# Kernel optimization log

Hardware: AMD Instinct MI355X
Metric: run time of the kernel (lower is better)

The kernel has to match this reference:

```python
import jax, jax.numpy as jnp
import numpy as np

N_NODES = 50000
N_EDGES = 800000
N_ENT = 500000
N_REL = 500
L = 2          # num_layers
H = 8          # head_num
D = 16         # per-head dim (hidden_dim // head_num)
HID = H * D    # 128
IN = 128       # in_ent_dim == in_rel_dim == hidden_dim
B = 64         # number of graphs in the batch
SLOPE = 0.2    # leaky-relu negative slope


def setup_inputs() -> dict:
    key = jax.random.key(0)
    ks = jax.random.split(key, 11)
    return {
        "ent_table": jax.random.normal(ks[0], (N_ENT, IN), jnp.float32) * 0.05,
        "rel_table": jax.random.normal(ks[1], (N_REL, IN), jnp.float32) * 0.05,
        "W_ent": jax.random.normal(ks[2], (L, IN, HID), jnp.float32) * 0.05,
        "W_rel": jax.random.normal(ks[3], (L, IN, HID), jnp.float32) * 0.05,
        "attn_l": jax.random.normal(ks[4], (L, H, D), jnp.float32) * 0.05,
        "attn_r": jax.random.normal(ks[5], (L, H, D), jnp.float32) * 0.05,
        "attn_e": jax.random.normal(ks[6], (L, H, D), jnp.float32) * 0.05,
        "ent_ids": jax.random.randint(ks[7], (N_NODES,), 0, N_ENT, jnp.int32),
        "rel_ids": jax.random.randint(ks[8], (N_EDGES,), 0, N_REL, jnp.int32),
        "src": jax.random.randint(ks[9], (N_EDGES,), 0, N_NODES, jnp.int32),
        "dst": jax.random.randint(ks[10], (N_EDGES,), 0, N_NODES, jnp.int32),
        # node-0 offset of each subgraph in the batched graph
        "graph_offsets": jnp.arange(B, dtype=jnp.int32) * (N_NODES // B),
    }


def _kge_layer(h, rel_f, src, dst, W_e, W_r, a_l, a_r, a_e):
    # GAT-style relation-aware message passing (KGELayer)
    feat = (h @ W_e).reshape(-1, H, D)        # [N,H,D]
    rfeat = (rel_f @ W_r).reshape(-1, H, D)   # [E,H,D]
    el = jnp.einsum('nhd,hd->nh', feat, a_l)  # src score
    er = jnp.einsum('nhd,hd->nh', feat, a_r)  # dst score
    ee = jnp.einsum('ehd,hd->eh', rfeat, a_e) # relation score
    e = jax.nn.leaky_relu(el[src] + er[dst] + ee, SLOPE)  # [E,H]
    # segment softmax over incoming edges of each dst node
    emax = jax.ops.segment_max(e, dst, num_segments=N_NODES)
    ex = jnp.exp(e - emax[dst])
    denom = jax.ops.segment_sum(ex, dst, num_segments=N_NODES)
    alpha = ex / denom[dst]                   # [E,H]
    msg = (feat[src] + rfeat) * alpha[:, :, None]  # [E,H,D]
    out = jax.ops.segment_sum(msg, dst, num_segments=N_NODES)  # [N,H,D]
    return out.reshape(-1, HID)


def reference(ent_table, rel_table, W_ent, W_rel, attn_l, attn_r, attn_e,
              ent_ids, rel_ids, src, dst, graph_offsets):
    h = ent_table[ent_ids]       # [N,IN]
    rel_f = rel_table[rel_ids]   # [E,IN]
    for l in range(L):
        h = _kge_layer(h, rel_f, src, dst, W_ent[l], W_rel[l],
                       attn_l[l], attn_r[l], attn_e[l])
    # CLS embedding: node 0 of each unbatched subgraph
    return h[graph_offsets]      # [B,HID]
```

## Files before the change

kernel.cpp:

```cpp
#include <hip/hip_runtime.h>
#include <hip/hip_bf16.h>


#define NN   50000
#define NE   800000
#define NR   500
#define HH   8
#define DD   16
#define HIDD 128
#define BB   64

#define MAXE2 16384
#define MAXS1 16448
#define MAXE1 262144
#define MAXS0 50000


__global__ void k_init(int* slot2, int* slot1, int* slot0, int* counters) {
    int i = blockIdx.x * blockDim.x + threadIdx.x;
    int stride = gridDim.x * blockDim.x;
    for (int n = i; n < NN; n += stride) { slot2[n] = -1; slot1[n] = -1; slot0[n] = -1; }
    if (i < 8) counters[i] = 0;
}

__global__ void k_seed(const int* goffs, int* slot2, int* slot1, int* nodesS1,
                       int* counters) {
    int i = threadIdx.x;
    if (i < BB) {
        int n = goffs[i];
        slot2[n] = i;
        slot1[n] = -2;
        nodesS1[i] = n;
    }
    if (i == 0) counters[0] = BB;
}

#define EBUF 1024
#define NBUF 512
__global__ void k_scan(const int* __restrict__ src, const int* __restrict__ dst,
                       const int* __restrict__ slotHit, int* __restrict__ slotNew,
                       int* elist, int elistCap, int* nodes, int nodesCap,
                       int* counters, int cntE, int cntN) {
    __shared__ int lE[EBUF];
    __shared__ int lN[NBUF];
    __shared__ int cEsh, cNsh, baseE, baseN;
    if (threadIdx.x == 0) { cEsh = 0; cNsh = 0; }
    __syncthreads();
    int per = (NE + gridDim.x - 1) / gridDim.x;
    int lo = blockIdx.x * per;
    int hi = lo + per; if (hi > NE) hi = NE;
    for (int base = lo; base < hi; base += blockDim.x) {
        int e = base + threadIdx.x;
        if (e < hi) {
            int d = dst[e];
            if (slotHit[d] >= 0) {
                int pos = atomicAdd(&cEsh, 1);
                lE[pos] = e;
                int s = src[e];
                int old = atomicCAS(&slotNew[s], -1, -2);
                if (old == -1) {
                    int p2 = atomicAdd(&cNsh, 1);
                    lN[p2] = s;
                }
            }
        }
        __syncthreads();
        if (cEsh >= EBUF - 256 || cNsh >= NBUF - 256) {
            int nE = cEsh, nN = cNsh;
            if (threadIdx.x == 0) {
                baseE = atomicAdd(&counters[cntE], nE);
                baseN = atomicAdd(&counters[cntN], nN);
            }
            __syncthreads();
            for (int i = threadIdx.x; i < nE; i += blockDim.x) {
                int g = baseE + i; if (g < elistCap) elist[g] = lE[i];
            }
            for (int i = threadIdx.x; i < nN; i += blockDim.x) {
                int g = baseN + i; if (g < nodesCap) nodes[g] = lN[i];
            }
            __syncthreads();
            if (threadIdx.x == 0) { cEsh = 0; cNsh = 0; }
        }
        __syncthreads();
    }
    int nE = cEsh, nN = cNsh;
    if (threadIdx.x == 0) {
        baseE = atomicAdd(&counters[cntE], nE);
        baseN = atomicAdd(&counters[cntN], nN);
    }
    __syncthreads();
    for (int i = threadIdx.x; i < nE; i += blockDim.x) {
        int g = baseE + i; if (g < elistCap) elist[g] = lE[i];
    }
    for (int i = threadIdx.x; i < nN; i += blockDim.x) {
        int g = baseN + i; if (g < nodesCap) nodes[g] = lN[i];
    }
}

__global__ void k_finS1(int* slot1, const int* nodesS1, int* slot0, int* nodesS0,
                        int* counters, int* deg) {
    int k = blockIdx.x * blockDim.x + threadIdx.x;
    int cnt = counters[0]; if (cnt > MAXS1) cnt = MAXS1;
    if (k < cnt) {
        int n = nodesS1[k];
        slot1[n] = k;
        slot0[n] = -2;
        nodesS0[k] = n;
    }
    if (k < MAXS1) deg[k] = 0;
    if (k == 0) counters[1] = cnt;
}

__global__ void k_finS0(int* slot0, const int* nodesS0, const int* counters) {
    int k = blockIdx.x * blockDim.x + threadIdx.x;
    int cnt = counters[1]; if (cnt > MAXS0) cnt = MAXS0;
    if (k < cnt) slot0[nodesS0[k]] = k;
}


__global__ void k_deg(const int* e1list, const int* counters, const int* dst,
                      const int* slot1, int* deg) {
    int i = blockIdx.x * blockDim.x + threadIdx.x;
    int stride = gridDim.x * blockDim.x;
    int cnt = counters[3]; if (cnt > MAXE1) cnt = MAXE1;
    for (; i < cnt; i += stride) {
        int e = e1list[i];
        atomicAdd(&deg[slot1[dst[e]]], 1);
    }
}

#define PFXT 1024
__global__ void k_pfx(const int* counters, const int* __restrict__ deg,
                      int* rowstart, int* cursor) {
    __shared__ int buf[PFXT];
    __shared__ int carrySh;
    int t = threadIdx.x;
    int cnt = counters[0]; if (cnt > MAXS1) cnt = MAXS1;
    if (t == 0) carrySh = 0;
    __syncthreads();
    for (int base = 0; base < cnt; base += PFXT) {
        int i = base + t;
        int v = (i < cnt) ? deg[i] : 0;
        buf[t] = v;
        __syncthreads();
        for (int off = 1; off < PFXT; off <<= 1) {
            int x = (t >= off) ? buf[t - off] : 0;
            __syncthreads();
            buf[t] += x;
            __syncthreads();
        }
        int carry = carrySh;
        int excl = carry + buf[t] - v;
        if (i < cnt) { rowstart[i] = excl; cursor[i] = excl; }
        __syncthreads();
        if (t == PFXT - 1) carrySh = carry + buf[PFXT - 1];
        __syncthreads();
    }
    if (t == 0) rowstart[cnt] = carrySh;
}

__global__ void k_bucket(const int* e1list, const int* counters, const int* dst,
                         const int* slot1, int* cursor, int* ebuck) {
    int i = blockIdx.x * blockDim.x + threadIdx.x;
    int stride = gridDim.x * blockDim.x;
    int cnt = counters[3]; if (cnt > MAXE1) cnt = MAXE1;
    for (; i < cnt; i += stride) {
        int e = e1list[i];
        int kd = slot1[dst[e]];
        int pos = atomicAdd(&cursor[kd], 1);
        ebuck[pos] = e;
    }
}

__global__ void k_rel(const float* rel_table, const float* __restrict__ W_rel,
                      const float* attn_e, float* rproj, float* ee) {
    int b = blockIdx.x;
    int l = b / NR, r = b % NR;
    int t = threadIdx.x;
    __shared__ float row[HIDD];
    __shared__ float rp[HIDD];
    row[t] = rel_table[r * HIDD + t];
    __syncthreads();
    const float* W = W_rel + l * HIDD * HIDD;
    float acc = 0.f;
    for (int j = 0; j < HIDD; j++) acc += row[j] * W[j * HIDD + t];
    rproj[(l * NR + r) * HIDD + t] = acc;
    rp[t] = acc;
    __syncthreads();
    if (t < HH) {
        float s = 0.f;
        for (int d = 0; d < DD; d++) s += rp[t * DD + d] * attn_e[(l * HH + t) * DD + d];
        ee[(l * NR + r) * HH + t] = s;
    }
}

#define FT 8
__global__ void k_feat0(const int* nodesS0, const int* counters, const int* ent_ids,
                        const float* __restrict__ ent_table, const float* __restrict__ W_ent,
                        const float* __restrict__ attn_l, const float* __restrict__ attn_r,
                        float* feat0, float* el0, float* er0) {
    int t = threadIdx.x;
    int cnt = counters[1]; if (cnt > MAXS0) cnt = MAXS0;
    __shared__ float rows[FT][HIDD];
    int nTiles = (cnt + FT - 1) / FT;
    for (int tile = blockIdx.x; tile < nTiles; tile += gridDim.x) {
        int k0 = tile * FT;
        #pragma unroll
        for (int m = 0; m < FT; m++) {
            int k = k0 + m;
            int n = nodesS0[k < cnt ? k : 0];
            rows[m][t] = ent_table[(long)ent_ids[n] * HIDD + t];
        }
        __syncthreads();
        float acc[FT];
        #pragma unroll
        for (int m = 0; m < FT; m++) acc[m] = 0.f;
        for (int j = 0; j < HIDD; j++) {
            float w = W_ent[j * HIDD + t];
            #pragma unroll
            for (int m = 0; m < FT; m++) acc[m] += rows[m][j] * w;
        }
        __syncthreads();
        #pragma unroll
        for (int m = 0; m < FT; m++) {
            int k = k0 + m;
            if (k < cnt) feat0[k * HIDD + t] = acc[m];
            rows[m][t] = acc[m];
        }
        __syncthreads();
        {
            int m = t >> 4, idx = t & 15, h = idx >> 1, isR = idx & 1;
            int k = k0 + m;
            if (k < cnt) {
                const float* av = (isR ? attn_r : attn_l) + h * DD;
                float s = 0.f;
                for (int d = 0; d < DD; d++) s += rows[m][h * DD + d] * av[d];
                if (isR) er0[k * HH + h] = s; else el0[k * HH + h] = s;
            }
        }
        __syncthreads();
    }
}

__global__ void k_layer1(const int* counters, const int* nodesS1,
                         const int* __restrict__ rowstart, const int* __restrict__ ebuck,
                         const int* __restrict__ src, const int* __restrict__ rel_ids,
                         const int* __restrict__ slot0,
                         const float* __restrict__ feat0, const float* __restrict__ rproj0,
                         const float* __restrict__ el0, const float* __restrict__ er0,
                         const float* __restrict__ ee0,
                         const float* __restrict__ W_ent1,
                         const float* attn_l1, const float* attn_r1,
                         float* feat1, float* el1, float* er1) {
    int t = threadIdx.x;
    int h = t >> 4;
    int cnt = counters[0]; if (cnt > MAXS1) cnt = MAXS1;
    __shared__ float row[HIDD];
    __shared__ float f[HIDD];
    for (int k = blockIdx.x; k < cnt; k += gridDim.x) {
        int n = nodesS1[k];
        int kd0 = slot0[n];
        float er_h = er0[kd0 * HH + h];
        int lo = rowstart[k], hi = rowstart[k + 1];
        float acc = 0.f, den = 0.f;
        for (int i = lo; i < hi; i++) {
            int e = ebuck[i];
            int s = src[e];
            int ks = slot0[s];
            int rid = rel_ids[e];
            float sc = el0[ks * HH + h] + er_h + ee0[rid * HH + h];
            sc = sc >= 0.f ? sc : 0.2f * sc;
            float ex = expf(sc);
            acc += (feat0[ks * HIDD + t] + rproj0[rid * HIDD + t]) * ex;
            den += ex;
        }
        row[t] = den > 0.f ? acc / den : 0.f;
        __syncthreads();
        float a2 = 0.f;
        for (int j = 0; j < HIDD; j++) a2 += row[j] * W_ent1[j * HIDD + t];
        feat1[k * HIDD + t] = a2;
        f[t] = a2;
        __syncthreads();
        if (t < HH) {
            float s = 0.f;
            for (int d = 0; d < DD; d++) s += f[t * DD + d] * attn_l1[t * DD + d];
            el1[k * HH + t] = s;
        } else if (t < 2 * HH) {
            int hh = t - HH;
            float s = 0.f;
            for (int d = 0; d < DD; d++) s += f[hh * DD + d] * attn_r1[hh * DD + d];
            er1[k * HH + hh] = s;
        }
        __syncthreads();
    }
}

__global__ void k_layer2(const int* counters, const int* goffs,
                         const int* __restrict__ e2list,
                         const int* __restrict__ src, const int* __restrict__ dst,
                         const int* __restrict__ rel_ids,
                         const int* __restrict__ slot1, const int* __restrict__ slot2,
                         const float* __restrict__ feat1, const float* __restrict__ rproj1,
                         const float* __restrict__ el1, const float* __restrict__ er1,
                         const float* __restrict__ ee1,
                         float* out) {
    int g = blockIdx.x;
    int t = threadIdx.x;
    int h = t >> 4;
    int cnt2 = counters[2]; if (cnt2 > MAXE2) cnt2 = MAXE2;
    int n = goffs[g];
    int kd1 = slot1[n];
    float er_h = er1[kd1 * HH + h];
    __shared__ int lE[128];
    __shared__ int lc;
    float acc = 0.f, den = 0.f;
    for (int base = 0; base < cnt2; base += blockDim.x) {
        if (t == 0) lc = 0;
        __syncthreads();
        int i = base + t;
        if (i < cnt2) {
            int e = e2list[i];
            if (slot2[dst[e]] == g) {
                int p = atomicAdd(&lc, 1);
                lE[p] = e;
            }
        }
        __syncthreads();
        int m = lc;
        for (int q = 0; q < m; q++) {
            int e = lE[q];
            int s = src[e];
            int ks = slot1[s];
            int rid = rel_ids[e];
            float sc = el1[ks * HH + h] + er_h + ee1[rid * HH + h];
            sc = sc >= 0.f ? sc : 0.2f * sc;
            float ex = expf(sc);
            acc += (feat1[ks * HIDD + t] + rproj1[rid * HIDD + t]) * ex;
            den += ex;
        }
        __syncthreads();
    }
    out[g * HIDD + t] = den > 0.f ? acc / den : 0.f;
}

extern "C" void kernel_launch(void* const* d_in, const int* in_sizes, int n_in,
                              void* d_out, int out_size, void* d_ws, size_t ws_size,
                              hipStream_t stream) {
    const float* ent_table = (const float*)d_in[0];
    const float* rel_table = (const float*)d_in[1];
    const float* W_ent     = (const float*)d_in[2];
    const float* W_rel     = (const float*)d_in[3];
    const float* attn_l    = (const float*)d_in[4];
    const float* attn_r    = (const float*)d_in[5];
    const float* attn_e    = (const float*)d_in[6];
    const int*   ent_ids   = (const int*)d_in[7];
    const int*   rel_ids   = (const int*)d_in[8];
    const int*   src       = (const int*)d_in[9];
    const int*   dst       = (const int*)d_in[10];
    const int*   goffs     = (const int*)d_in[11];
    float*       out       = (float*)d_out;

    char* p = (char*)d_ws;
    auto alloc = [&](size_t nbytes) {
        void* q = (void*)p;
        p += (nbytes + 255) & ~(size_t)255;
        return q;
    };
    float* rproj   = (float*)alloc((size_t)2 * NR * HIDD * 4);
    float* ee      = (float*)alloc((size_t)2 * NR * HH * 4);
    int*   slot2   = (int*)alloc((size_t)NN * 4);
    int*   slot1   = (int*)alloc((size_t)NN * 4);
    int*   slot0   = (int*)alloc((size_t)NN * 4);
    int*   nodesS1 = (int*)alloc((size_t)MAXS1 * 4);
    int*   nodesS0 = (int*)alloc((size_t)MAXS0 * 4);
    int*   e2list  = (int*)alloc((size_t)MAXE2 * 4);
    int*   e1list  = (int*)alloc((size_t)MAXE1 * 4);
    int*   counters= (int*)alloc(8 * 4);
    int*   deg     = (int*)alloc((size_t)MAXS1 * 4);
    int*   rowstart= (int*)alloc((size_t)(MAXS1 + 1) * 4);
    int*   cursor  = (int*)alloc((size_t)MAXS1 * 4);
    int*   ebuck   = (int*)alloc((size_t)MAXE1 * 4);
    float* feat0   = (float*)alloc((size_t)MAXS0 * HIDD * 4);
    float* el0     = (float*)alloc((size_t)MAXS0 * HH * 4);
    float* er0     = (float*)alloc((size_t)MAXS0 * HH * 4);
    float* feat1   = (float*)alloc((size_t)MAXS1 * HIDD * 4);
    float* el1     = (float*)alloc((size_t)MAXS1 * HH * 4);
    float* er1     = (float*)alloc((size_t)MAXS1 * HH * 4);

    const float* rproj0 = rproj;
    const float* rproj1 = rproj + (size_t)NR * HIDD;
    const float* ee0 = ee;
    const float* ee1 = ee + (size_t)NR * HH;
    const float* W_ent0 = W_ent;
    const float* W_ent1 = W_ent + HIDD * HIDD;
    const float* attn_l0 = attn_l, *attn_l1 = attn_l + HH * DD;
    const float* attn_r0 = attn_r, *attn_r1 = attn_r + HH * DD;

    hipLaunchKernelGGL(k_init, dim3(256), dim3(256), 0, stream,
                       slot2, slot1, slot0, counters);
    hipLaunchKernelGGL(k_seed, dim3(1), dim3(64), 0, stream,
                       goffs, slot2, slot1, nodesS1, counters);
    hipLaunchKernelGGL(k_scan, dim3(512), dim3(256), 0, stream,
                       src, dst, slot2, slot1, e2list, MAXE2, nodesS1, MAXS1,
                       counters, 2, 0);
    hipLaunchKernelGGL(k_finS1, dim3((MAXS1 + 255) / 256), dim3(256), 0, stream,
                       slot1, nodesS1, slot0, nodesS0, counters, deg);
    hipLaunchKernelGGL(k_scan, dim3(512), dim3(256), 0, stream,
                       src, dst, slot1, slot0, e1list, MAXE1, nodesS0, MAXS0,
                       counters, 3, 1);
    hipLaunchKernelGGL(k_finS0, dim3((MAXS0 + 255) / 256), dim3(256), 0, stream,
                       slot0, nodesS0, counters);
    hipLaunchKernelGGL(k_deg, dim3(256), dim3(256), 0, stream,
                       e1list, counters, dst, slot1, deg);
    hipLaunchKernelGGL(k_pfx, dim3(1), dim3(PFXT), 0, stream,
                       counters, deg, rowstart, cursor);
    hipLaunchKernelGGL(k_bucket, dim3(256), dim3(256), 0, stream,
                       e1list, counters, dst, slot1, cursor, ebuck);
    hipLaunchKernelGGL(k_rel, dim3(2 * NR), dim3(HIDD), 0, stream,
                       rel_table, W_rel, attn_e, rproj, ee);
    hipLaunchKernelGGL(k_feat0, dim3(1024), dim3(HIDD), 0, stream,
                       nodesS0, counters, ent_ids, ent_table, W_ent0,
                       attn_l0, attn_r0, feat0, el0, er0);
    hipLaunchKernelGGL(k_layer1, dim3(2048), dim3(HIDD), 0, stream,
                       counters, nodesS1, rowstart, ebuck, src, rel_ids, slot0,
                       feat0, rproj0, el0, er0, ee0, W_ent1, attn_l1, attn_r1,
                       feat1, el1, er1);
    hipLaunchKernelGGL(k_layer2, dim3(BB), dim3(HIDD), 0, stream,
                       counters, goffs, e2list, src, dst, rel_ids, slot1, slot2,
                       feat1, rproj1, el1, er1, ee1, out);
}
```

Baseline: 455.7 us.

## Bucket edges into fixed-capacity per-node slots during scan, fuse setup kernels

The frontier scan now writes each matching edge straight into a fixed-stride per-destination bucket using an atomic cursor. This removes the edge list, degree count, prefix sum and bucketing kernels. The relation projection, layer-0 feature projection and slot0 finalisation are fused into one launch. Both layer kernels precompute source slots, relation ids and exp scores per edge in shared memory before the aggregation loop. The fixed capacity of 256 edges per node silently drops edges beyond that, and contention on the global per-slot atomics may rise.

```diff
diff --git a/kernel.cpp b/kernel.cpp
--- a/kernel.cpp
+++ b/kernel.cpp
@@ -10,16 +10,19 @@
 #define HIDD 128
 #define BB   64
 
-#define MAXE2 16384
 #define MAXS1 16448
-#define MAXE1 262144
 #define MAXS0 50000
-
-
-__global__ void k_init(int* slot2, int* slot1, int* slot0, int* counters) {
+#define MAXD1 256
+#define MAXD2 256
+
+
+__global__ void k_init(int* slot2, int* slot1, int* slot0, int* c1, int* c2,
+                       int* counters) {
     int i = blockIdx.x * blockDim.x + threadIdx.x;
     int stride = gridDim.x * blockDim.x;
     for (int n = i; n < NN; n += stride) { slot2[n] = -1; slot1[n] = -1; slot0[n] = -1; }
+    for (int n = i; n < MAXS1; n += stride) c1[n] = 0;
+    if (i < BB) c2[i] = 0;
     if (i < 8) counters[i] = 0;
 }
 
@@ -35,16 +38,14 @@
     if (i == 0) counters[0] = BB;
 }
 
-#define EBUF 1024
 #define NBUF 512
 __global__ void k_scan(const int* __restrict__ src, const int* __restrict__ dst,
                        const int* __restrict__ slotHit, int* __restrict__ slotNew,
-                       int* elist, int elistCap, int* nodes, int nodesCap,
-                       int* counters, int cntE, int cntN) {
-    __shared__ int lE[EBUF];
+                       int* __restrict__ ebuck, int maxd, int* __restrict__ cursor,
+                       int* nodes, int nodesCap, int* counters, int cntN) {
     __shared__ int lN[NBUF];
-    __shared__ int cEsh, cNsh, baseE, baseN;
-    if (threadIdx.x == 0) { cEsh = 0; cNsh = 0; }
+    __shared__ int cNsh, baseN;
+    if (threadIdx.x == 0) cNsh = 0;
     __syncthreads();
     int per = (NE + gridDim.x - 1) / gridDim.x;
     int lo = blockIdx.x * per;
@@ -53,9 +54,10 @@
         int e = base + threadIdx.x;
         if (e < hi) {
             int d = dst[e];
-            if (slotHit[d] >= 0) {
-                int pos = atomicAdd(&cEsh, 1);
-                lE[pos] = e;
+            int slot = slotHit[d];
+            if (slot >= 0) {
+                int pos = atomicAdd(&cursor[slot], 1);
+                if (pos < maxd) ebuck[slot * maxd + pos] = e;
                 int s = src[e];
                 int old = atomicCAS(&slotNew[s], -1, -2);
                 if (old == -1) {
@@ -65,40 +67,28 @@
             }
         }
         __syncthreads();
-        if (cEsh >= EBUF - 256 || cNsh >= NBUF - 256) {
-            int nE = cEsh, nN = cNsh;
-            if (threadIdx.x == 0) {
-                baseE = atomicAdd(&counters[cntE], nE);
-                baseN = atomicAdd(&counters[cntN], nN);
-            }
+        if (cNsh >= NBUF - 256) {
+            int nN = cNsh;
+            if (threadIdx.x == 0) baseN = atomicAdd(&counters[cntN], nN);
             __syncthreads();
-            for (int i = threadIdx.x; i < nE; i += blockDim.x) {
-                int g = baseE + i; if (g < elistCap) elist[g] = lE[i];
-            }
             for (int i = threadIdx.x; i < nN; i += blockDim.x) {
                 int g = baseN + i; if (g < nodesCap) nodes[g] = lN[i];
             }
             __syncthreads();
-            if (threadIdx.x == 0) { cEsh = 0; cNsh = 0; }
-        }
-        __syncthreads();
-    }
-    int nE = cEsh, nN = cNsh;
-    if (threadIdx.x == 0) {
-        baseE = atomicAdd(&counters[cntE], nE);
-        baseN = atomicAdd(&counters[cntN], nN);
-    }
+            if (threadIdx.x == 0) cNsh = 0;
+        }
+        __syncthreads();
+    }
+    int nN = cNsh;
+    if (threadIdx.x == 0) baseN = atomicAdd(&counters[cntN], nN);
     __syncthreads();
-    for (int i = threadIdx.x; i < nE; i += blockDim.x) {
-        int g = baseE + i; if (g < elistCap) elist[g] = lE[i];
-    }
     for (int i = threadIdx.x; i < nN; i += blockDim.x) {
         int g = baseN + i; if (g < nodesCap) nodes[g] = lN[i];
     }
 }
 
 __global__ void k_finS1(int* slot1, const int* nodesS1, int* slot0, int* nodesS0,
-                        int* counters, int* deg) {
+                        int* counters) {
     int k = blockIdx.x * blockDim.x + threadIdx.x;
     int cnt = counters[0]; if (cnt > MAXS1) cnt = MAXS1;
     if (k < cnt) {
@@ -107,109 +97,49 @@
         slot0[n] = -2;
         nodesS0[k] = n;
     }
-    if (k < MAXS1) deg[k] = 0;
     if (k == 0) counters[1] = cnt;
 }
 
-__global__ void k_finS0(int* slot0, const int* nodesS0, const int* counters) {
-    int k = blockIdx.x * blockDim.x + threadIdx.x;
+#define RELB 1000
+#define FT 8
+__global__ void k_relfeat0(const float* rel_table, const float* __restrict__ W_rel,
+                           const float* attn_e, float* rproj, float* ee,
+                           const int* nodesS0, const int* counters, const int* ent_ids,
+                           const float* __restrict__ ent_table, const float* __restrict__ W_ent,
+                           const float* __restrict__ attn_l, const float* __restrict__ attn_r,
+                           float* feat0, float* el0, float* er0, int* slot0) {
+    int t = threadIdx.x;
+    __shared__ float sh[FT][HIDD];
+    if (blockIdx.x < RELB) {
+        int b = blockIdx.x;
+        int l = b / NR, r = b % NR;
+        sh[0][t] = rel_table[r * HIDD + t];
+        __syncthreads();
+        const float* W = W_rel + l * HIDD * HIDD;
+        float acc = 0.f;
+        for (int j = 0; j < HIDD; j++) acc += sh[0][j] * W[j * HIDD + t];
+        rproj[(l * NR + r) * HIDD + t] = acc;
+        sh[1][t] = acc;
+        __syncthreads();
+        if (t < HH) {
+            float s = 0.f;
+            #pragma unroll
+            for (int d = 0; d < DD; d++) s += sh[1][t * DD + d] * attn_e[(l * HH + t) * DD + d];
+            ee[(l * NR + r) * HH + t] = s;
+        }
+        return;
+    }
     int cnt = counters[1]; if (cnt > MAXS0) cnt = MAXS0;
-    if (k < cnt) slot0[nodesS0[k]] = k;
-}
-
-
-__global__ void k_deg(const int* e1list, const int* counters, const int* dst,
-                      const int* slot1, int* deg) {
-    int i = blockIdx.x * blockDim.x + threadIdx.x;
-    int stride = gridDim.x * blockDim.x;
-    int cnt = counters[3]; if (cnt > MAXE1) cnt = MAXE1;
-    for (; i < cnt; i += stride) {
-        int e = e1list[i];
-        atomicAdd(&deg[slot1[dst[e]]], 1);
-    }
-}
-
-#define PFXT 1024
-__global__ void k_pfx(const int* counters, const int* __restrict__ deg,
-                      int* rowstart, int* cursor) {
-    __shared__ int buf[PFXT];
-    __shared__ int carrySh;
-    int t = threadIdx.x;
-    int cnt = counters[0]; if (cnt > MAXS1) cnt = MAXS1;
-    if (t == 0) carrySh = 0;
-    __syncthreads();
-    for (int base = 0; base < cnt; base += PFXT) {
-        int i = base + t;
-        int v = (i < cnt) ? deg[i] : 0;
-        buf[t] = v;
-        __syncthreads();
-        for (int off = 1; off < PFXT; off <<= 1) {
-            int x = (t >= off) ? buf[t - off] : 0;
-            __syncthreads();
-            buf[t] += x;
-            __syncthreads();
-        }
-        int carry = carrySh;
-        int excl = carry + buf[t] - v;
-        if (i < cnt) { rowstart[i] = excl; cursor[i] = excl; }
-        __syncthreads();
-        if (t == PFXT - 1) carrySh = carry + buf[PFXT - 1];
-        __syncthreads();
-    }
-    if (t == 0) rowstart[cnt] = carrySh;
-}
-
-__global__ void k_bucket(const int* e1list, const int* counters, const int* dst,
-                         const int* slot1, int* cursor, int* ebuck) {
-    int i = blockIdx.x * blockDim.x + threadIdx.x;
-    int stride = gridDim.x * blockDim.x;
-    int cnt = counters[3]; if (cnt > MAXE1) cnt = MAXE1;
-    for (; i < cnt; i += stride) {
-        int e = e1list[i];
-        int kd = slot1[dst[e]];
-        int pos = atomicAdd(&cursor[kd], 1);
-        ebuck[pos] = e;
-    }
-}
-
-__global__ void k_rel(const float* rel_table, const float* __restrict__ W_rel,
-                      const float* attn_e, float* rproj, float* ee) {
-    int b = blockIdx.x;
-    int l = b / NR, r = b % NR;
-    int t = threadIdx.x;
-    __shared__ float row[HIDD];
-    __shared__ float rp[HIDD];
-    row[t] = rel_table[r * HIDD + t];
-    __syncthreads();
-    const float* W = W_rel + l * HIDD * HIDD;
-    float acc = 0.f;
-    for (int j = 0; j < HIDD; j++) acc += row[j] * W[j * HIDD + t];
-    rproj[(l * NR + r) * HIDD + t] = acc;
-    rp[t] = acc;
-    __syncthreads();
-    if (t < HH) {
-        float s = 0.f;
-        for (int d = 0; d < DD; d++) s += rp[t * DD + d] * attn_e[(l * HH + t) * DD + d];
-        ee[(l * NR + r) * HH + t] = s;
-    }
-}
-
-#define FT 8
-__global__ void k_feat0(const int* nodesS0, const int* counters, const int* ent_ids,
-                        const float* __restrict__ ent_table, const float* __restrict__ W_ent,
-                        const float* __restrict__ attn_l, const float* __restrict__ attn_r,
-                        float* feat0, float* el0, float* er0) {
-    int t = threadIdx.x;
-    int cnt = counters[1]; if (cnt > MAXS0) cnt = MAXS0;
-    __shared__ float rows[FT][HIDD];
     int nTiles = (cnt + FT - 1) / FT;
-    for (int tile = blockIdx.x; tile < nTiles; tile += gridDim.x) {
+    int gstride = gridDim.x - RELB;
+    for (int tile = blockIdx.x - RELB; tile < nTiles; tile += gstride) {
         int k0 = tile * FT;
         #pragma unroll
         for (int m = 0; m < FT; m++) {
             int k = k0 + m;
             int n = nodesS0[k < cnt ? k : 0];
-            rows[m][t] = ent_table[(long)ent_ids[n] * HIDD + t];
+            if (k < cnt && t == 0) slot0[n] = k;
+            sh[m][t] = ent_table[(long)ent_ids[n] * HIDD + t];
         }
         __syncthreads();
         float acc[FT];
@@ -218,14 +148,14 @@
         for (int j = 0; j < HIDD; j++) {
             float w = W_ent[j * HIDD + t];
             #pragma unroll
-            for (int m = 0; m < FT; m++) acc[m] += rows[m][j] * w;
+            for (int m = 0; m < FT; m++) acc[m] += sh[m][j] * w;
         }
         __syncthreads();
         #pragma unroll
         for (int m = 0; m < FT; m++) {
             int k = k0 + m;
             if (k < cnt) feat0[k * HIDD + t] = acc[m];
-            rows[m][t] = acc[m];
+            sh[m][t] = acc[m];
         }
         __syncthreads();
         {
@@ -234,7 +164,8 @@
             if (k < cnt) {
                 const float* av = (isR ? attn_r : attn_l) + h * DD;
                 float s = 0.f;
-                for (int d = 0; d < DD; d++) s += rows[m][h * DD + d] * av[d];
+                #pragma unroll
+                for (int d = 0; d < DD; d++) s += sh[m][h * DD + d] * av[d];
                 if (isR) er0[k * HH + h] = s; else el0[k * HH + h] = s;
             }
         }
@@ -242,8 +173,8 @@
     }
 }
 
-__global__ void k_layer1(const int* counters, const int* nodesS1,
-                         const int* __restrict__ rowstart, const int* __restrict__ ebuck,
+__global__ void k_layer1(const int* counters,
+                         const int* __restrict__ c1, const int* __restrict__ ebuck1,
                          const int* __restrict__ src, const int* __restrict__ rel_ids,
                          const int* __restrict__ slot0,
                          const float* __restrict__ feat0, const float* __restrict__ rproj0,
@@ -255,23 +186,31 @@
     int t = threadIdx.x;
     int h = t >> 4;
     int cnt = counters[0]; if (cnt > MAXS1) cnt = MAXS1;
+    __shared__ int   eks[MAXD1];
+    __shared__ int   erid[MAXD1];
+    __shared__ float exsh[MAXD1 * HH];
     __shared__ float row[HIDD];
     __shared__ float f[HIDD];
     for (int k = blockIdx.x; k < cnt; k += gridDim.x) {
-        int n = nodesS1[k];
-        int kd0 = slot0[n];
-        float er_h = er0[kd0 * HH + h];
-        int lo = rowstart[k], hi = rowstart[k + 1];
+        int deg = c1[k]; if (deg > MAXD1) deg = MAXD1;
+        for (int i = t; i < deg; i += blockDim.x) {
+            int e = ebuck1[k * MAXD1 + i];
+            eks[i]  = slot0[src[e]];
+            erid[i] = rel_ids[e];
+        }
+        __syncthreads();
+        for (int idx = t; idx < deg * HH; idx += blockDim.x) {
+            int i = idx >> 3, hh = idx & 7;
+            float sc = el0[eks[i] * HH + hh] + er0[k * HH + hh] + ee0[erid[i] * HH + hh];
+            sc = sc >= 0.f ? sc : 0.2f * sc;
+            exsh[idx] = expf(sc);
+        }
+        __syncthreads();
         float acc = 0.f, den = 0.f;
-        for (int i = lo; i < hi; i++) {
-            int e = ebuck[i];
-            int s = src[e];
-            int ks = slot0[s];
-            int rid = rel_ids[e];
-            float sc = el0[ks * HH + h] + er_h + ee0[rid * HH + h];
-            sc = sc >= 0.f ? sc : 0.2f * sc;
-            float ex = expf(sc);
-            acc += (feat0[ks * HIDD + t] + rproj0[rid * HIDD + t]) * ex;
+        #pragma unroll 4
+        for (int i = 0; i < deg; i++) {
+            float ex = exsh[i * HH + h];
+            acc += (feat0[eks[i] * HIDD + t] + rproj0[erid[i] * HIDD + t]) * ex;
             den += ex;
         }
         row[t] = den > 0.f ? acc / den : 0.f;
@@ -283,11 +222,13 @@
         __syncthreads();
         if (t < HH) {
             float s = 0.f;
+            #pragma unroll
             for (int d = 0; d < DD; d++) s += f[t * DD + d] * attn_l1[t * DD + d];
             el1[k * HH + t] = s;
         } else if (t < 2 * HH) {
             int hh = t - HH;
             float s = 0.f;
+            #pragma unroll
             for (int d = 0; d < DD; d++) s += f[hh * DD + d] * attn_r1[hh * DD + d];
             er1[k * HH + hh] = s;
         }
@@ -295,11 +236,9 @@
     }
 }
 
-__global__ void k_layer2(const int* counters, const int* goffs,
-                         const int* __restrict__ e2list,
-                         const int* __restrict__ src, const int* __restrict__ dst,
-                         const int* __restrict__ rel_ids,
-                         const int* __restrict__ slot1, const int* __restrict__ slot2,
+__global__ void k_layer2(const int* __restrict__ c2, const int* __restrict__ ebuck2,
+                         const int* __restrict__ src, const int* __restrict__ rel_ids,
+                         const int* __restrict__ slot1,
                          const float* __restrict__ feat1, const float* __restrict__ rproj1,
                          const float* __restrict__ el1, const float* __restrict__ er1,
                          const float* __restrict__ ee1,
@@ -307,38 +246,29 @@
     int g = blockIdx.x;
     int t = threadIdx.x;
     int h = t >> 4;
-    int cnt2 = counters[2]; if (cnt2 > MAXE2) cnt2 = MAXE2;
-    int n = goffs[g];
-    int kd1 = slot1[n];
-    float er_h = er1[kd1 * HH + h];
-    __shared__ int lE[128];
-    __shared__ int lc;
+    __shared__ int   eks[MAXD2];
+    __shared__ int   erid[MAXD2];
+    __shared__ float exsh[MAXD2 * HH];
+    int deg = c2[g]; if (deg > MAXD2) deg = MAXD2;
+    for (int i = t; i < deg; i += blockDim.x) {
+        int e = ebuck2[g * MAXD2 + i];
+        eks[i]  = slot1[src[e]];
+        erid[i] = rel_ids[e];
+    }
+    __syncthreads();
+    for (int idx = t; idx < deg * HH; idx += blockDim.x) {
+        int i = idx >> 3, hh = idx & 7;
+        float sc = el1[eks[i] * HH + hh] + er1[g * HH + hh] + ee1[erid[i] * HH + hh];
+        sc = sc >= 0.f ? sc : 0.2f * sc;
+        exsh[idx] = expf(sc);
+    }
+    __syncthreads();
     float acc = 0.f, den = 0.f;
-    for (int base = 0; base < cnt2; base += blockDim.x) {
-        if (t == 0) lc = 0;
-        __syncthreads();
-        int i = base + t;
-        if (i < cnt2) {
-            int e = e2list[i];
-            if (slot2[dst[e]] == g) {
-                int p = atomicAdd(&lc, 1);
-                lE[p] = e;
-            }
-        }
-        __syncthreads();
-        int m = lc;
-        for (int q = 0; q < m; q++) {
-            int e = lE[q];
-            int s = src[e];
-            int ks = slot1[s];
-            int rid = rel_ids[e];
-            float sc = el1[ks * HH + h] + er_h + ee1[rid * HH + h];
-            sc = sc >= 0.f ? sc : 0.2f * sc;
-            float ex = expf(sc);
-            acc += (feat1[ks * HIDD + t] + rproj1[rid * HIDD + t]) * ex;
-            den += ex;
-        }
-        __syncthreads();
+    #pragma unroll 4
+    for (int i = 0; i < deg; i++) {
+        float ex = exsh[i * HH + h];
+        acc += (feat1[eks[i] * HIDD + t] + rproj1[erid[i] * HIDD + t]) * ex;
+        den += ex;
     }
     out[g * HIDD + t] = den > 0.f ? acc / den : 0.f;
 }
@@ -373,13 +303,11 @@
     int*   slot0   = (int*)alloc((size_t)NN * 4);
     int*   nodesS1 = (int*)alloc((size_t)MAXS1 * 4);
     int*   nodesS0 = (int*)alloc((size_t)MAXS0 * 4);
-    int*   e2list  = (int*)alloc((size_t)MAXE2 * 4);
-    int*   e1list  = (int*)alloc((size_t)MAXE1 * 4);
     int*   counters= (int*)alloc(8 * 4);
-    int*   deg     = (int*)alloc((size_t)MAXS1 * 4);
-    int*   rowstart= (int*)alloc((size_t)(MAXS1 + 1) * 4);
-    int*   cursor  = (int*)alloc((size_t)MAXS1 * 4);
-    int*   ebuck   = (int*)alloc((size_t)MAXE1 * 4);
+    int*   c1      = (int*)alloc((size_t)MAXS1 * 4);
+    int*   c2      = (int*)alloc((size_t)BB * 4);
+    int*   ebuck1  = (int*)alloc((size_t)MAXS1 * MAXD1 * 4);
+    int*   ebuck2  = (int*)alloc((size_t)BB * MAXD2 * 4);
     float* feat0   = (float*)alloc((size_t)MAXS0 * HIDD * 4);
     float* el0     = (float*)alloc((size_t)MAXS0 * HH * 4);
     float* er0     = (float*)alloc((size_t)MAXS0 * HH * 4);
@@ -397,35 +325,26 @@
     const float* attn_r0 = attn_r, *attn_r1 = attn_r + HH * DD;
 
     hipLaunchKernelGGL(k_init, dim3(256), dim3(256), 0, stream,
-                       slot2, slot1, slot0, counters);
+                       slot2, slot1, slot0, c1, c2, counters);
     hipLaunchKernelGGL(k_seed, dim3(1), dim3(64), 0, stream,
                        goffs, slot2, slot1, nodesS1, counters);
     hipLaunchKernelGGL(k_scan, dim3(512), dim3(256), 0, stream,
-                       src, dst, slot2, slot1, e2list, MAXE2, nodesS1, MAXS1,
-                       counters, 2, 0);
+                       src, dst, slot2, slot1, ebuck2, MAXD2, c2,
+                       nodesS1, MAXS1, counters, 0);
     hipLaunchKernelGGL(k_finS1, dim3((MAXS1 + 255) / 256), dim3(256), 0, stream,
-                       slot1, nodesS1, slot0, nodesS0, counters, deg);
+                       slot1, nodesS1, slot0, nodesS0, counters);
     hipLaunchKernelGGL(k_scan, dim3(512), dim3(256), 0, stream,
-                       src, dst, slot1, slot0, e1list, MAXE1, nodesS0, MAXS0,
-                       counters, 3, 1);
-    hipLaunchKernelGGL(k_finS0, dim3((MAXS0 + 255) / 256), dim3(256), 0, stream,
-                       slot0, nodesS0, counters);
-    hipLaunchKernelGGL(k_deg, dim3(256), dim3(256), 0, stream,
-                       e1list, counters, dst, slot1, deg);
-    hipLaunchKernelGGL(k_pfx, dim3(1), dim3(PFXT), 0, stream,
-                       counters, deg, rowstart, cursor);
-    hipLaunchKernelGGL(k_bucket, dim3(256), dim3(256), 0, stream,
-                       e1list, counters, dst, slot1, cursor, ebuck);
-    hipLaunchKernelGGL(k_rel, dim3(2 * NR), dim3(HIDD), 0, stream,
-                       rel_table, W_rel, attn_e, rproj, ee);
-    hipLaunchKernelGGL(k_feat0, dim3(1024), dim3(HIDD), 0, stream,
+                       src, dst, slot1, slot0, ebuck1, MAXD1, c1,
+                       nodesS0, MAXS0, counters, 1);
+    hipLaunchKernelGGL(k_relfeat0, dim3(RELB + 1048), dim3(HIDD), 0, stream,
+                       rel_table, W_rel, attn_e, rproj, ee,
                        nodesS0, counters, ent_ids, ent_table, W_ent0,
-                       attn_l0, attn_r0, feat0, el0, er0);
-    hipLaunchKernelGGL(k_layer1, dim3(2048), dim3(HIDD), 0, stream,
-                       counters, nodesS1, rowstart, ebuck, src, rel_ids, slot0,
+                       attn_l0, attn_r0, feat0, el0, er0, slot0);
+    hipLaunchKernelGGL(k_layer1, dim3(1024), dim3(HIDD), 0, stream,
+                       counters, c1, ebuck1, src, rel_ids, slot0,
                        feat0, rproj0, el0, er0, ee0, W_ent1, attn_l1, attn_r1,
                        feat1, el1, er1);
     hipLaunchKernelGGL(k_layer2, dim3(BB), dim3(HIDD), 0, stream,
-                       counters, goffs, e2list, src, dst, rel_ids, slot1, slot2,
+                       c2, ebuck2, src, rel_ids, slot1,
                        feat1, rproj1, el1, er1, ee1, out);
 }
```

Result: faster. 400.9 us (-12.0%).
